# Kernel tuning notes

Hardware: AMD Instinct MI355X
Metric: run time of the kernel (lower is better)

Reference implementation:

```python
import jax, jax.numpy as jnp
import numpy as np

B = 2
H_GRID, W_GRID, RADIUS = 48, 48, 3
D_MODEL, N_HEADS, D_HEAD = 512, 8, 64
N = H_GRID * W_GRID          # 2304 tokens
WSIZE = (2 * RADIUS + 1) ** 2  # 49 neighbors per token
D_ACT = D_HEAD                # d_head even -> d_act = d_head
SCALE = D_ACT ** -0.5
NEG = -1e9


def _grid_neighbors():
    rr = np.arange(N) // W_GRID
    cc = np.arange(N) % W_GRID
    off = np.arange(-RADIUS, RADIUS + 1)
    dr, dc = np.meshgrid(off, off, indexing='ij')
    dr, dc = dr.ravel(), dc.ravel()
    nr = rr[:, None] + dr[None, :]
    nc = cc[:, None] + dc[None, :]
    valid = (nr >= 0) & (nr < H_GRID) & (nc >= 0) & (nc < W_GRID)
    idx = np.clip(nr, 0, H_GRID - 1) * W_GRID + np.clip(nc, 0, W_GRID - 1)
    pos = np.stack([rr, cc], axis=-1).astype(np.float32)
    return idx.astype(np.int32), valid, pos


def setup_inputs() -> dict:
    key = jax.random.key(0)
    ks = jax.random.split(key, 8)
    idx, valid, pos = _grid_neighbors()
    s = D_MODEL ** -0.5
    return {
        'x': jax.random.normal(ks[0], (B, N, D_MODEL), jnp.float32),
        'positions': jnp.asarray(pos),
        'W_Q': jax.random.normal(ks[1], (D_MODEL, N_HEADS * D_HEAD), jnp.float32) * s,
        'W_K': jax.random.normal(ks[2], (D_MODEL, N_HEADS * D_HEAD), jnp.float32) * s,
        'W_V': jax.random.normal(ks[3], (D_MODEL, N_HEADS * D_HEAD), jnp.float32) * s,
        'W_O': jax.random.normal(ks[4], (N_HEADS * D_HEAD, D_MODEL), jnp.float32) * s,
        # learnable active-subspace basis per head (near-identity init, QR'd in fwd)
        'U': jnp.eye(D_HEAD, D_ACT)[None] + 0.05 * jax.random.normal(ks[5], (N_HEADS, D_HEAD, D_ACT), jnp.float32),
        # per-head rotation generator frequencies: theta = dr . freqs per 2x2 block
        'freqs': 0.5 * jax.random.normal(ks[6], (N_HEADS, 2, D_HEAD // 2), jnp.float32),
        'neighbor_index': jnp.asarray(idx),
        'neighbor_mask': jnp.asarray(valid),
    }


def reference(x, positions, W_Q, W_K, W_V, W_O, U, freqs, neighbor_index, neighbor_mask):
    Bt, Nt, _ = x.shape

    def heads(h):  # (B,N,H*d) -> (B,H,N,d)
        return h.reshape(Bt, Nt, N_HEADS, D_HEAD).transpose(0, 2, 1, 3)

    Q = heads(x @ W_Q)
    K = heads(x @ W_K)
    V = heads(x @ W_V)

    # Active subspace projection Pi_act = U_ortho U_ortho^T, applied as x@U@U^T
    U_ortho = jnp.linalg.qr(U)[0]                       # (H, d, d_act)
    Q = jnp.einsum('bhnd,hde,hfe->bhnf', Q, U_ortho, U_ortho)
    K = jnp.einsum('bhnd,hde,hfe->bhnf', K, U_ortho, U_ortho)

    # per-(i,j) relative rotation: block-diagonal 2x2 rotations with
    # angles theta[h,n,w,p] = (r_j - r_i) . freqs[h,:,p]
    drel = positions[neighbor_index] - positions[:, None, :]   # (N,W,2)
    theta = jnp.einsum('nwc,hcp->hnwp', drel, freqs)           # (H,N,W,d/2)
    cos, sin = jnp.cos(theta), jnp.sin(theta)

    K_loc = K[:, :, neighbor_index]                            # (B,H,N,W,d) gather
    Ke, Ko = K_loc[..., 0::2], K_loc[..., 1::2]
    Kr_e = cos[None] * Ke - sin[None] * Ko
    Kr_o = sin[None] * Ke + cos[None] * Ko
    K_rot = jnp.stack([Kr_e, Kr_o], axis=-1).reshape(K_loc.shape)

    scores = jnp.einsum('bhnd,bhnwd->bhnw', Q, K_rot) * SCALE
    scores = jnp.where(neighbor_mask[None, None], scores, NEG)
    w = jax.nn.softmax(scores, axis=-1)

    V_loc = V[:, :, neighbor_index]                            # (B,H,N,W,d)
    out = jnp.einsum('bhnw,bhnwd->bhnd', w, V_loc)
    out = out.transpose(0, 2, 1, 3).reshape(Bt, Nt, N_HEADS * D_HEAD)
    return out @ W_O
```

## Files before the change

kernel.cpp:

```cpp
#include <hip/hip_runtime.h>
#include <math.h>


#define BB 2
#define HGRID 48
#define WGRID 48
#define NNODE (HGRID*WGRID)
#define RAD 3
#define WSZ 49
#define DMODEL 512
#define NHEAD 8
#define SCALE 0.125f
#define MROWS (BB*NNODE)
#define TPAD 141

typedef _Float16 f16;
typedef __attribute__((ext_vector_type(8))) _Float16 f16x8;
typedef __attribute__((ext_vector_type(2))) _Float16 h2;
typedef __attribute__((ext_vector_type(4))) float f32x4;

typedef union { f16x8 v8; h2 h[4]; } pack8;

#if __has_builtin(__builtin_amdgcn_fdot2)
__device__ __forceinline__ float fdot2(h2 a, h2 b, float c) {
    return __builtin_amdgcn_fdot2(a, b, c, false);
}
#else
__device__ __forceinline__ float fdot2(h2 a, h2 b, float c) {
    return fmaf((float)a.x, (float)b.x, fmaf((float)a.y, (float)b.y, c));
}
#endif

__global__ void convert_all(const float* __restrict__ x,
                            const float* __restrict__ WQ, const float* __restrict__ WK,
                            const float* __restrict__ WV, const float* __restrict__ WO,
                            f16* __restrict__ x2, f16* __restrict__ Wall) {
    int id = blockIdx.x * 256 + threadIdx.x;
    if (id < MROWS * 64) {
        int r = id >> 6, c8 = (id & 63) << 3;
        float4 a = *(const float4*)&x[(size_t)r * 512 + c8];
        float4 b = *(const float4*)&x[(size_t)r * 512 + c8 + 4];
        f16 o[8] = {(f16)a.x, (f16)a.y, (f16)a.z, (f16)a.w,
                    (f16)b.x, (f16)b.y, (f16)b.z, (f16)b.w};
        *(f16x8*)&x2[(size_t)r * 512 + c8] = *(f16x8*)o;
        return;
    }
    id -= MROWS * 64;
    if (id >= 2048 * 64) return;
    const int kb = ((id >> 6) & 63) << 3;
    const int np = (id & 63) + ((id >> 12) << 6);
    const float* S;
    int n;
    if (np < 1536) { int t = np >> 9; n = np & 511; S = (t == 0) ? WQ : (t == 1) ? WK : WV; }
    else           { n = np - 1536;  S = WO; }
    f16 o[8];
#pragma unroll
    for (int i = 0; i < 8; ++i) o[i] = (f16)S[(size_t)(kb + i) * 512 + n];
    *(f16x8*)&Wall[(size_t)np * 512 + kb] = *(f16x8*)o;
}

__global__ __launch_bounds__(256)
void mgemm0(const f16* __restrict__ A, const f16* __restrict__ Bt,
            f16* __restrict__ Qh, f16* __restrict__ Kh, f16* __restrict__ Vh,
            const float* __restrict__ freqs) {
    __shared__ f16 As[128 * 64];
    __shared__ f16 Bs[128 * 64];

    const int tid = threadIdx.x;
    const int l = tid & 63, wid = tid >> 6;

    const int bid = blockIdx.x;
    const int swz = (bid & 7) * 54 + (bid >> 3);
    const int m0 = (swz / 12) * 128;
    const int n0 = (swz % 12) * 128;

    const int wm = (wid >> 1) * 64, wn = (wid & 1) * 64;
    const int fr = l & 15, fk = l >> 4;
    const int srow = l >> 3, slot = l & 7;

    f32x4 acc[4][4];
#pragma unroll
    for (int m = 0; m < 4; ++m)
#pragma unroll
        for (int n = 0; n < 4; ++n) acc[m][n] = (f32x4){0.f, 0.f, 0.f, 0.f};

    for (int kt = 0; kt < 8; ++kt) {
        const int k0 = kt * 64;
#pragma unroll
        for (int j = 0; j < 4; ++j) {
            const int r = wid * 32 + j * 8 + srow;
            const int cA = (slot ^ (r & 7)) * 8;
            const f16* gA = A + (size_t)(m0 + r) * 512 + k0 + cA;
            __builtin_amdgcn_global_load_lds(
                (const __attribute__((address_space(1))) unsigned int*)gA,
                (__attribute__((address_space(3))) unsigned int*)(As + wid * 2048 + j * 512),
                16, 0, 0);
            const f16* gB = Bt + (size_t)(n0 + r) * 512 + k0 + cA;
            __builtin_amdgcn_global_load_lds(
                (const __attribute__((address_space(1))) unsigned int*)gB,
                (__attribute__((address_space(3))) unsigned int*)(Bs + wid * 2048 + j * 512),
                16, 0, 0);
        }
        asm volatile("s_waitcnt vmcnt(0)" ::: "memory");
        __syncthreads();

        f16x8 af[4][2], bfr[4][2];
#pragma unroll
        for (int m = 0; m < 4; ++m) {
            const int row = wm + m * 16 + fr;
#pragma unroll
            for (int kk = 0; kk < 2; ++kk) {
                const int b = (kk * 64 + fk * 16) ^ ((row & 7) << 4);
                af[m][kk] = *(const f16x8*)((const char*)As + row * 128 + b);
            }
        }
#pragma unroll
        for (int n = 0; n < 4; ++n) {
            const int row = wn + n * 16 + fr;
#pragma unroll
            for (int kk = 0; kk < 2; ++kk) {
                const int b = (kk * 64 + fk * 16) ^ ((row & 7) << 4);
                bfr[n][kk] = *(const f16x8*)((const char*)Bs + row * 128 + b);
            }
        }
#pragma unroll
        for (int kk = 0; kk < 2; ++kk)
#pragma unroll
            for (int m = 0; m < 4; ++m)
#pragma unroll
                for (int n = 0; n < 4; ++n)
                    acc[m][n] = __builtin_amdgcn_mfma_f32_16x16x32_f16(
                        af[m][kk], bfr[n][kk], acc[m][n], 0, 0, 0);
        __syncthreads();
    }

#pragma unroll
    for (int nf = 0; nf < 4; ++nf) {
        const int ccol = n0 + wn + nf * 16 + fr;
        const int t = ccol >> 9;
        const int h = (ccol >> 6) & 7;
        const int d = ccol & 63;
        const int p = d >> 1;
        f16* Cp = (t == 0) ? Qh : (t == 1) ? Kh : Vh;
        if (t < 2) {
            const float fR = freqs[h * 64 + p];
            const float fC = freqs[h * 64 + 32 + p];
            const float sgn = (d & 1) ? 1.0f : -1.0f;
            float sF, cF;
            __sincosf(fC, &sF, &cF);
#pragma unroll
            for (int mf = 0; mf < 4; ++mf) {
                const int g0r = m0 + wm + mf * 16 + fk * 4;
                const int b_ = g0r >= NNODE;
                const int nn0 = g0r - b_ * NNODE;
                const int rr = nn0 / WGRID;
                const int cc0 = nn0 - rr * WGRID;
                float sn, cs;
                __sincosf((float)rr * fR + (float)cc0 * fC, &sn, &cs);
                const size_t base = ((size_t)((b_ * NHEAD + h) * NNODE + nn0)) * 64 + d;
#pragma unroll
                for (int i = 0; i < 4; ++i) {
                    float val = acc[mf][nf][i];
                    float part = __shfl_xor(val, 1);
                    float outv = fmaf(sgn * part, sn, val * cs);
                    Cp[base + (size_t)i * 64] = (f16)outv;
                    float cs2 = cs * cF - sn * sF;
                    sn = sn * cF + cs * sF;
                    cs = cs2;
                }
            }
        } else {
#pragma unroll
            for (int mf = 0; mf < 4; ++mf) {
#pragma unroll
                for (int i = 0; i < 4; ++i) {
                    const int grow = m0 + wm + mf * 16 + fk * 4 + i;
                    const int b_ = grow >= NNODE;
                    const int nn = grow - b_ * NNODE;
                    Cp[((size_t)((b_ * NHEAD + h) * NNODE + nn)) * 64 + d] =
                        (f16)acc[mf][nf][i];
                }
            }
        }
    }
}

__global__ __launch_bounds__(256)
void mgemm1(const f16* __restrict__ A, const f16* __restrict__ Bt,
            float* __restrict__ Cf) {
    __shared__ f16 As[64 * 64];
    __shared__ f16 Bs[128 * 64];

    const int tid = threadIdx.x;
    const int l = tid & 63, wid = tid >> 6;

    const int bid = blockIdx.x;
    const int swz = (bid & 7) * 36 + (bid >> 3);
    const int m0 = (swz >> 2) * 64;
    const int n0 = (swz & 3) * 128;

    const int wm = (wid >> 1) * 32, wn = (wid & 1) * 64;
    const int fr = l & 15, fk = l >> 4;
    const int srow = l >> 3, slot = l & 7;

    f32x4 acc[2][4];
#pragma unroll
    for (int m = 0; m < 2; ++m)
#pragma unroll
        for (int n = 0; n < 4; ++n) acc[m][n] = (f32x4){0.f, 0.f, 0.f, 0.f};

    for (int kt = 0; kt < 8; ++kt) {
        const int k0 = kt * 64;
#pragma unroll
        for (int j = 0; j < 2; ++j) {
            const int r = wid * 16 + j * 8 + srow;
            const int cA = (slot ^ (r & 7)) * 8;
            const f16* gA = A + (size_t)(m0 + r) * 512 + k0 + cA;
            __builtin_amdgcn_global_load_lds(
                (const __attribute__((address_space(1))) unsigned int*)gA,
                (__attribute__((address_space(3))) unsigned int*)(As + wid * 1024 + j * 512),
                16, 0, 0);
        }
#pragma unroll
        for (int j = 0; j < 4; ++j) {
            const int r = wid * 32 + j * 8 + srow;
            const int cA = (slot ^ (r & 7)) * 8;
            const f16* gB = Bt + (size_t)(n0 + r) * 512 + k0 + cA;
            __builtin_amdgcn_global_load_lds(
                (const __attribute__((address_space(1))) unsigned int*)gB,
                (__attribute__((address_space(3))) unsigned int*)(Bs + wid * 2048 + j * 512),
                16, 0, 0);
        }
        asm volatile("s_waitcnt vmcnt(0)" ::: "memory");
        __syncthreads();

        f16x8 af[2][2], bfr[4][2];
#pragma unroll
        for (int m = 0; m < 2; ++m) {
            const int row = wm + m * 16 + fr;
#pragma unroll
            for (int kk = 0; kk < 2; ++kk) {
                const int b = (kk * 64 + fk * 16) ^ ((row & 7) << 4);
                af[m][kk] = *(const f16x8*)((const char*)As + row * 128 + b);
            }
        }
#pragma unroll
        for (int n = 0; n < 4; ++n) {
            const int row = wn + n * 16 + fr;
#pragma unroll
            for (int kk = 0; kk < 2; ++kk) {
                const int b = (kk * 64 + fk * 16) ^ ((row & 7) << 4);
                bfr[n][kk] = *(const f16x8*)((const char*)Bs + row * 128 + b);
            }
        }
#pragma unroll
        for (int kk = 0; kk < 2; ++kk)
#pragma unroll
            for (int m = 0; m < 2; ++m)
#pragma unroll
                for (int n = 0; n < 4; ++n)
                    acc[m][n] = __builtin_amdgcn_mfma_f32_16x16x32_f16(
                        af[m][kk], bfr[n][kk], acc[m][n], 0, 0, 0);
        __syncthreads();
    }

#pragma unroll
    for (int nf = 0; nf < 4; ++nf) {
        const int ccol = n0 + wn + nf * 16 + fr;
#pragma unroll
        for (int mf = 0; mf < 2; ++mf) {
#pragma unroll
            for (int i = 0; i < 4; ++i) {
                const int grow = m0 + wm + mf * 16 + fk * 4 + i;
                Cf[(size_t)grow * 512 + ccol] = acc[mf][nf][i];
            }
        }
    }
}

__global__ __launch_bounds__(256, 4)
void attn7(const f16* __restrict__ Qh, const f16* __restrict__ Kh,
           const f16* __restrict__ Vh, f16* __restrict__ out2) {
    __shared__ h2 T[32 * TPAD];

    const int tid = threadIdx.x;
    const int wid = tid >> 6, lane = tid & 63;
    const int qs = lane >> 3, wg = lane & 7;

    const int bid = blockIdx.x;
    const int t  = bid % 72, bh = bid / 72;
    const int tr = t % 12,   tc = t / 12;
    const int r0 = tr * 4,   c0 = tc * 8;
    const int h  = bh & 7,   b_ = bh >> 3;

    const int lr0 = max(0, r0 - 3), lr1 = min(HGRID - 1, r0 + 6);
    const int lc0 = max(0, c0 - 3), lc1 = min(WGRID - 1, c0 + 10);
    const int NR = lr1 - lr0 + 1, NC = lc1 - lc0 + 1;

    const f16* Kb = Kh + (size_t)bh * NNODE * 64;
    const f16* Vb = Vh + (size_t)bh * NNODE * 64;

    const int rq = r0 + wid, cq = c0 + qs;
    const int nq = rq * WGRID + cq;
    const f16* qrow = Qh + ((size_t)bh * NNODE + nq) * 64;
    h2 q2[32];
#pragma unroll
    for (int j8 = 0; j8 < 8; ++j8) {
        pack8 v;
        v.v8 = *(const f16x8*)&qrow[j8 * 8];
#pragma unroll
        for (int k = 0; k < 4; ++k) q2[j8 * 4 + k] = v.h[k];
    }

    const int cnt = NR * NC * 8;

    f16x8 vpre[5];
#pragma unroll
    for (int s = 0; s < 5; ++s) {
        const int i = tid + s * 256;
        if (i < cnt) {
            const int row = i >> 3, p4 = i & 7;
            const int glr = row / NC, glc = row - glr * NC;
            const int n = (lr0 + glr) * WGRID + (lc0 + glc);
            vpre[s] = *(const f16x8*)&Vb[(size_t)n * 64 + p4 * 8];
        }
    }

    for (int i = tid; i < cnt; i += 256) {
        const int row = i >> 3, p4 = i & 7;
        const int glr = row / NC, glc = row - glr * NC;
        const int n = (lr0 + glr) * WGRID + (lc0 + glc);
        pack8 v;
        v.v8 = *(const f16x8*)&Kb[(size_t)n * 64 + p4 * 8];
#pragma unroll
        for (int j = 0; j < 4; ++j) T[(p4 * 4 + j) * TPAD + row] = v.h[j];
    }
    __syncthreads();

    float sc[7], es[7];
    float mx = -1e30f;
#pragma unroll
    for (int k = 0; k < 7; ++k) {
        const int w = wg + 8 * k;
        sc[k] = -1e30f;
        if (w < WSZ) {
            const int dr = w / 7 - RAD, dc = w % 7 - RAD;
            const int nr = rq + dr, nc = cq + dc;
            const bool valid = ((unsigned)nr < (unsigned)HGRID) &&
                               ((unsigned)nc < (unsigned)WGRID);
            const int nrl = min(max(nr, lr0), lr1) - lr0;
            const int ncl = min(max(nc, lc0), lc1) - lc0;
            const int row = nrl * NC + ncl;
            float s = 0.0f;
#pragma unroll
            for (int j = 0; j < 32; ++j) s = fdot2(q2[j], T[j * TPAD + row], s);
            sc[k] = valid ? s * SCALE : -1e9f;
            mx = fmaxf(mx, sc[k]);
        }
    }
#pragma unroll
    for (int o = 1; o < 8; o <<= 1) mx = fmaxf(mx, __shfl_xor(mx, o));
    float sum = 0.0f;
#pragma unroll
    for (int k = 0; k < 7; ++k) {
        const int w = wg + 8 * k;
        es[k] = 0.0f;
        if (w < WSZ) { es[k] = __expf(sc[k] - mx); sum += es[k]; }
    }
#pragma unroll
    for (int o = 1; o < 8; o <<= 1) sum += __shfl_xor(sum, o);
    const float inv = 1.0f / sum;
    float esn[7];
#pragma unroll
    for (int k = 0; k < 7; ++k) esn[k] = es[k] * inv;

    __syncthreads();

#pragma unroll
    for (int s = 0; s < 5; ++s) {
        const int i = tid + s * 256;
        if (i < cnt) {
            const int row = i >> 3, p4 = i & 7;
            pack8 v; v.v8 = vpre[s];
#pragma unroll
            for (int j = 0; j < 4; ++j) T[(p4 * 4 + j) * TPAD + row] = v.h[j];
        }
    }
    __syncthreads();

    const int dg = wg;
    float2 acc[4] = {{0, 0}, {0, 0}, {0, 0}, {0, 0}};
#pragma unroll
    for (int w = 0; w < WSZ; ++w) {
        const int dr = w / 7 - RAD, dc = w % 7 - RAD;
        const int nr = rq + dr, nc = cq + dc;
        const int nrl = min(max(nr, lr0), lr1) - lr0;
        const int ncl = min(max(nc, lc0), lc1) - lc0;
        const int row = nrl * NC + ncl;
        const float pw = __shfl(esn[w >> 3], (lane & 0x38) | (w & 7));
#pragma unroll
        for (int j = 0; j < 4; ++j) {
            h2 v2 = T[(dg * 4 + j) * TPAD + row];
            acc[j].x = fmaf(pw, (float)v2.x, acc[j].x);
            acc[j].y = fmaf(pw, (float)v2.y, acc[j].y);
        }
    }

    f16 o[8] = {(f16)acc[0].x, (f16)acc[0].y, (f16)acc[1].x, (f16)acc[1].y,
                (f16)acc[2].x, (f16)acc[2].y, (f16)acc[3].x, (f16)acc[3].y};
    const size_t rowb = (size_t)(b_ * NNODE + nq) * 512 + h * 64 + dg * 8;
    *(f16x8*)&out2[rowb] = *(f16x8*)o;
}

extern "C" void kernel_launch(void* const* d_in, const int* in_sizes, int n_in,
                              void* d_out, int out_size, void* d_ws, size_t ws_size,
                              hipStream_t stream) {
    const float* x     = (const float*)d_in[0];
    const float* WQ    = (const float*)d_in[2];
    const float* WK    = (const float*)d_in[3];
    const float* WV    = (const float*)d_in[4];
    const float* WO    = (const float*)d_in[5];
    const float* freqs = (const float*)d_in[7];

    const size_t HN = (size_t)16 * NNODE * 64;
    f16* Qh   = (f16*)d_ws;
    f16* Kh   = Qh + HN;
    f16* Vh   = Kh + HN;
    f16* x2   = Vh + HN;
    f16* Wall = x2 + (size_t)MROWS * 512;
    f16* Wo2  = Wall + (size_t)1536 * 512;

    convert_all<<<((MROWS + 2048) * 64 + 255) / 256, 256, 0, stream>>>(
        x, WQ, WK, WV, WO, x2, Wall);

    mgemm0<<<432, 256, 0, stream>>>(x2, Wall, Qh, Kh, Vh, freqs);

    attn7<<<16 * 72, 256, 0, stream>>>(Qh, Kh, Vh, x2);

    mgemm1<<<288, 256, 0, stream>>>(x2, Wo2, (float*)d_out);
}
```

Before: 56.25 us.

## Store K/V tiles row-major in LDS and read them with 128-bit vector loads

Replaces the dimension-major transposed LDS staging of the K and V neighbourhood tiles with a row-per-token layout using a padded row stride. Tiles are written and read with 128-bit vector accesses, both in the score dot products and in the V accumulation, instead of scalar h2 accesses. The goal is fewer LDS instructions and no scattered transposing stores. The indexing leaves half of each row unused, so the LDS footprint roughly doubles to about 40 KB per block, which may cut resident blocks per CU and could change bank-conflict behaviour.

```diff
diff --git a/kernel.cpp b/kernel.cpp
--- a/kernel.cpp
+++ b/kernel.cpp
@@ -12,7 +12,7 @@
 #define NHEAD 8
 #define SCALE 0.125f
 #define MROWS (BB*NNODE)
-#define TPAD 141
+#define TROW 72
 
 typedef _Float16 f16;
 typedef __attribute__((ext_vector_type(8))) _Float16 f16x8;
@@ -279,9 +279,9 @@
 }
 
 __global__ __launch_bounds__(256, 4)
-void attn7(const f16* __restrict__ Qh, const f16* __restrict__ Kh,
+void attn8(const f16* __restrict__ Qh, const f16* __restrict__ Kh,
            const f16* __restrict__ Vh, f16* __restrict__ out2) {
-    __shared__ h2 T[32 * TPAD];
+    __shared__ h2 T[140 * TROW];
 
     const int tid = threadIdx.x;
     const int wid = tid >> 6, lane = tid & 63;
@@ -319,21 +319,18 @@
     for (int s = 0; s < 5; ++s) {
         const int i = tid + s * 256;
         if (i < cnt) {
-            const int row = i >> 3, p4 = i & 7;
+            const int row = i >> 3, seg = i & 7;
             const int glr = row / NC, glc = row - glr * NC;
             const int n = (lr0 + glr) * WGRID + (lc0 + glc);
-            vpre[s] = *(const f16x8*)&Vb[(size_t)n * 64 + p4 * 8];
+            vpre[s] = *(const f16x8*)&Vb[(size_t)n * 64 + seg * 8];
         }
     }
 
     for (int i = tid; i < cnt; i += 256) {
-        const int row = i >> 3, p4 = i & 7;
+        const int row = i >> 3, seg = i & 7;
         const int glr = row / NC, glc = row - glr * NC;
         const int n = (lr0 + glr) * WGRID + (lc0 + glc);
-        pack8 v;
-        v.v8 = *(const f16x8*)&Kb[(size_t)n * 64 + p4 * 8];
-#pragma unroll
-        for (int j = 0; j < 4; ++j) T[(p4 * 4 + j) * TPAD + row] = v.h[j];
+        *(f16x8*)&T[row * TROW + seg * 8] = *(const f16x8*)&Kb[(size_t)n * 64 + seg * 8];
     }
     __syncthreads();
 
@@ -353,7 +350,13 @@
             const int row = nrl * NC + ncl;
             float s = 0.0f;
 #pragma unroll
-            for (int j = 0; j < 32; ++j) s = fdot2(q2[j], T[j * TPAD + row], s);
+            for (int j8 = 0; j8 < 8; ++j8) {
+                pack8 kv;
+                kv.v8 = *(const f16x8*)&T[row * TROW + j8 * 8];
+#pragma unroll
+                for (int jj = 0; jj < 4; ++jj)
+                    s = fdot2(q2[j8 * 4 + jj], kv.h[jj], s);
+            }
             sc[k] = valid ? s * SCALE : -1e9f;
             mx = fmaxf(mx, sc[k]);
         }
@@ -380,10 +383,8 @@
     for (int s = 0; s < 5; ++s) {
         const int i = tid + s * 256;
         if (i < cnt) {
-            const int row = i >> 3, p4 = i & 7;
-            pack8 v; v.v8 = vpre[s];
-#pragma unroll
-            for (int j = 0; j < 4; ++j) T[(p4 * 4 + j) * TPAD + row] = v.h[j];
+            const int row = i >> 3, seg = i & 7;
+            *(f16x8*)&T[row * TROW + seg * 8] = vpre[s];
         }
     }
     __syncthreads();
@@ -398,11 +399,12 @@
         const int ncl = min(max(nc, lc0), lc1) - lc0;
         const int row = nrl * NC + ncl;
         const float pw = __shfl(esn[w >> 3], (lane & 0x38) | (w & 7));
+        pack8 vv;
+        vv.v8 = *(const f16x8*)&T[row * TROW + dg * 8];
 #pragma unroll
         for (int j = 0; j < 4; ++j) {
-            h2 v2 = T[(dg * 4 + j) * TPAD + row];
-            acc[j].x = fmaf(pw, (float)v2.x, acc[j].x);
-            acc[j].y = fmaf(pw, (float)v2.y, acc[j].y);
+            acc[j].x = fmaf(pw, (float)vv.h[j].x, acc[j].x);
+            acc[j].y = fmaf(pw, (float)vv.h[j].y, acc[j].y);
         }
     }
 
@@ -435,7 +437,7 @@
 
     mgemm0<<<432, 256, 0, stream>>>(x2, Wall, Qh, Kh, Vh, freqs);
 
-    attn7<<<16 * 72, 256, 0, stream>>>(Qh, Kh, Vh, x2);
+    attn8<<<16 * 72, 256, 0, stream>>>(Qh, Kh, Vh, x2);
 
     mgemm1<<<288, 256, 0, stream>>>(x2, Wo2, (float*)d_out);
 }
```

After: 56.32 us. No clear change (+0.1%).
